# Optimization experiments

Hardware: AMD Instinct MI355X
Metric: run time of the kernel (lower is better)

## Reference

```python
import jax, jax.numpy as jnp
import numpy as np

N_EMBD = 1024
N_HEAD = 16
B, T = 4, 2048

def setup_inputs() -> dict:
    key = jax.random.key(0)
    ks = jax.random.split(key, 5)
    C = N_EMBD
    s = 0.02
    return {
        "x": jax.random.normal(ks[0], (B, T, C), dtype=jnp.float32),
        "W_attn": jax.random.normal(ks[1], (C, 3 * C), dtype=jnp.float32) * s,
        "b_attn": jnp.zeros((3 * C,), dtype=jnp.float32),
        "W_proj": jax.random.normal(ks[2], (C, C), dtype=jnp.float32) * s,
        "b_proj": jnp.zeros((C,), dtype=jnp.float32),
    }

def reference(x, W_attn, b_attn, W_proj, b_proj):
    Bz, Tz, C = x.shape
    H = N_HEAD
    hd = C // H
    qkv = x @ W_attn + b_attn                      # [B,T,3C]
    q, k, v = jnp.split(qkv, 3, axis=-1)
    # [B,H,T,hd]
    q = q.reshape(Bz, Tz, H, hd).transpose(0, 2, 1, 3)
    k = k.reshape(Bz, Tz, H, hd).transpose(0, 2, 1, 3)
    v = v.reshape(Bz, Tz, H, hd).transpose(0, 2, 1, 3)
    att = jnp.einsum('bhqd,bhkd->bhqk', q, k) * (1.0 / np.sqrt(hd))
    causal = jnp.tril(jnp.ones((Tz, Tz), dtype=bool))
    att = jnp.where(causal, att, -jnp.inf)
    att = jax.nn.softmax(att, axis=-1)
    y = jnp.einsum('bhqk,bhkd->bhqd', att, v)      # [B,H,T,hd]
    y = y.transpose(0, 2, 1, 3).reshape(Bz, Tz, C)
    return y @ W_proj + b_proj
```

## Files before the change

kernel.cpp:

```cpp
#include <hip/hip_runtime.h>
#include <hip/hip_bf16.h>

#define NEMBD 1024
#define NHEAD 16
#define HD    64
#define BB    4
#define TT    2048
#define MM    (BB*TT)
#define NQKV  (3*NEMBD)

typedef unsigned short u16;
typedef __attribute__((ext_vector_type(8))) short short8;
typedef __attribute__((ext_vector_type(4))) float floatx4;
typedef __attribute__((ext_vector_type(16))) float floatx16;

__device__ __forceinline__ u16 f2bf(float f) {
    __hip_bfloat16 h = __float2bfloat16(f);
    return *reinterpret_cast<u16*>(&h);
}

__device__ __forceinline__ unsigned pack_bf16(float a, float b) {
    __hip_bfloat162 h2 = __float22bfloat162_rn(float2{a, b});
    return *reinterpret_cast<unsigned*>(&h2);
}

__device__ __forceinline__ unsigned trunc_pack(float a, float b) {
    return __builtin_amdgcn_perm(__float_as_uint(b), __float_as_uint(a), 0x07060302u);
}

__device__ __forceinline__ void gl_lds16(const u16* g, u16* l) {
    __builtin_amdgcn_global_load_lds(
        (const __attribute__((address_space(1))) unsigned int*)g,
        (__attribute__((address_space(3))) unsigned int*)l,
        16, 0, 0);
}

__device__ __forceinline__ short8 scale8(short8 f, float c) {
    union { short8 s; unsigned u[4]; } a, r;
    a.s = f;
    for (int i = 0; i < 4; i++) {
        float lo = __uint_as_float(a.u[i] << 16) * c;
        float hi = __uint_as_float(a.u[i] & 0xffff0000u) * c;
        r.u[i] = pack_bf16(lo, hi);
    }
    return r.s;
}

__global__ __launch_bounds__(256) void cast_f32_bf16(const float* __restrict__ in,
                                                     u16* __restrict__ out, int n) {
    int i = (blockIdx.x * 256 + threadIdx.x) * 4;
    if (i < n) {
        float4 v = *(const float4*)(in + i);
        uint2 o;
        o.x = pack_bf16(v.x, v.y);
        o.y = pack_bf16(v.z, v.w);
        *(uint2*)(out + i) = o;
    }
}

__global__ __launch_bounds__(256) void transpose_cast(const float* __restrict__ in,
                                                      u16* __restrict__ out, int K, int N) {
    __shared__ float tile[32][33];
    int n0 = blockIdx.x * 32, k0 = blockIdx.y * 32;
    int tx = threadIdx.x, ty = threadIdx.y;
    for (int i = 0; i < 4; i++)
        tile[ty + i * 8][tx] = in[(k0 + ty + i * 8) * N + n0 + tx];
    __syncthreads();
    for (int i = 0; i < 4; i++)
        out[(n0 + ty + i * 8) * K + k0 + tx] = f2bf(tile[tx][ty + i * 8]);
}

template <int EPI>
__global__ __launch_bounds__(256)
void gemm_bt(const u16* __restrict__ A, const u16* __restrict__ Bt,
             const float* __restrict__ bias, void* __restrict__ out0,
             u16* __restrict__ outK, u16* __restrict__ outV) {
    const int K = NEMBD;
    __shared__ u16 As[128 * 64];
    __shared__ u16 Bs[128 * 64];
    int tid = threadIdx.x;
    int lane = tid & 63, w = tid >> 6;
    int l32 = lane & 31, lhi = lane >> 5;
    int wm = w >> 1, wn = w & 1;
    int bM = blockIdx.y * 128, bN = blockIdx.x * 128;

    floatx16 acc[2][2];
    for (int i = 0; i < 2; i++)
        for (int j = 0; j < 2; j++)
            acc[i][j] = (floatx16)(0.f);

    int srow = lane >> 3;
    int scol = ((lane & 7) ^ srow) * 8;
    const u16* Ag = A  + (size_t)(bM + w * 32 + srow) * K + scol;
    const u16* Bg = Bt + (size_t)(bN + w * 32 + srow) * K + scol;

    int physo[4];
    for (int kc = 0; kc < 4; kc++)
        physo[kc] = ((kc * 2 + lhi) ^ (lane & 7)) * 8;

    for (int k0 = 0; k0 < K; k0 += 64) {
        for (int i = 0; i < 4; i++) {
            gl_lds16(Ag + (size_t)i * 8 * K + k0, &As[(w * 32 + i * 8) * 64]);
            gl_lds16(Bg + (size_t)i * 8 * K + k0, &Bs[(w * 32 + i * 8) * 64]);
        }
        __syncthreads();
        for (int kc = 0; kc < 4; kc++) {
            short8 af[2], bf[2];
            for (int i = 0; i < 2; i++)
                af[i] = *(const short8*)&As[(wm * 64 + i * 32 + l32) * 64 + physo[kc]];
            for (int j = 0; j < 2; j++)
                bf[j] = *(const short8*)&Bs[(wn * 64 + j * 32 + l32) * 64 + physo[kc]];
            for (int i = 0; i < 2; i++)
                for (int j = 0; j < 2; j++)
                    acc[i][j] = __builtin_amdgcn_mfma_f32_32x32x16_bf16(af[i], bf[j], acc[i][j], 0, 0, 0);
        }
        __syncthreads();
    }

    for (int j = 0; j < 2; j++) {
        int n = bN + wn * 64 + j * 32 + l32;
        float bv = bias[n];
        for (int i = 0; i < 2; i++) {
            int mbase = bM + wm * 64 + i * 32 + 4 * lhi;
            for (int reg = 0; reg < 16; reg++) {
                float v = acc[i][j][reg] + bv;
                int mg = mbase + (reg & 3) + 8 * (reg >> 2);
                if (EPI == 0) {
                    int which = n >> 10, c = n & 1023;
                    int h = c >> 6, d = c & 63;
                    int b = mg >> 11, t = mg & 2047;
                    u16* dst = (which == 0) ? (u16*)out0 : (which == 1 ? outK : outV);
                    dst[(((size_t)(b * NHEAD + h) * TT) + t) * HD + d] = f2bf(v);
                } else {
                    ((float*)out0)[(size_t)mg * NEMBD + n] = v;
                }
            }
        }
    }
}

__global__ __launch_bounds__(256, 2)
void attn_kernel(const u16* __restrict__ Q, const u16* __restrict__ Kg,
                 const u16* __restrict__ V, u16* __restrict__ Y) {
    __shared__ u16 Ks[64][72];
    __shared__ u16 Vt[64][72];
    __shared__ u16 Ps[4][32][72];

    int tid = threadIdx.x;
    int lane = tid & 63, w = tid >> 6;
    int quad = lane >> 4, l16 = lane & 15;
    int bh = blockIdx.x;
    int jq = blockIdx.y;
    int q0 = jq * 128;
    const u16* Qb = Q  + (size_t)bh * TT * HD;
    const u16* Kb = Kg + (size_t)bh * TT * HD;
    const u16* Vb = V  + (size_t)bh * TT * HD;
    int wq = q0 + w * 32;

    const float C = 0.18033688f;

    short8 qf[2][2];
    for (int qt = 0; qt < 2; qt++)
        for (int kd = 0; kd < 2; kd++)
            qf[qt][kd] = scale8(*(const short8*)(Qb + (size_t)(wq + qt * 16 + l16) * HD + kd * 32 + quad * 8), C);

    floatx4 o[4][2];
    for (int dt = 0; dt < 4; dt++)
        for (int qt = 0; qt < 2; qt++)
            o[dt][qt] = (floatx4){0.f, 0.f, 0.f, 0.f};
    float l_s[2] = {0.f, 0.f};

    int krow = tid >> 2, kcg = (tid & 3) * 16;
    int vkp = (tid & 31) * 2, vd0 = (tid >> 5) * 8;

    auto stage_write = [&](uint4 k0v, uint4 k1v, uint4 v0, uint4 v1) {
        *(uint4*)&Ks[krow][kcg]     = k0v;
        *(uint4*)&Ks[krow][kcg + 8] = k1v;
        const unsigned* w0p = (const unsigned*)&v0;
        const unsigned* w1p = (const unsigned*)&v1;
        for (int e = 0; e < 4; e++) {
            *(unsigned*)&Vt[vd0 + 2 * e][vkp]     = __builtin_amdgcn_perm(w1p[e], w0p[e], 0x05040100u);
            *(unsigned*)&Vt[vd0 + 2 * e + 1][vkp] = __builtin_amdgcn_perm(w1p[e], w0p[e], 0x07060302u);
        }
    };

    auto process = [&](int k0) {
        short8 kf[4][2];
        for (int kt = 0; kt < 4; kt++)
            for (int kd = 0; kd < 2; kd++)
                kf[kt][kd] = *(const short8*)&Ks[kt * 16 + l16][kd * 32 + quad * 8];

        floatx4 s[2][4];
        for (int qt = 0; qt < 2; qt++)
            for (int kt = 0; kt < 4; kt++) {
                floatx4 a = (floatx4){0.f, 0.f, 0.f, 0.f};
                a = __builtin_amdgcn_mfma_f32_16x16x32_bf16(kf[kt][0], qf[qt][0], a, 0, 0, 0);
                a = __builtin_amdgcn_mfma_f32_16x16x32_bf16(kf[kt][1], qf[qt][1], a, 0, 0, 0);
                s[qt][kt] = a;
            }

        bool diag = (k0 + 64 > wq);
        for (int qt = 0; qt < 2; qt++) {
            int qg = wq + qt * 16 + l16;
            if (diag) {
                for (int kt = 0; kt < 4; kt++)
                    for (int r = 0; r < 4; r++)
                        if (k0 + kt * 16 + quad * 4 + r > qg) s[qt][kt][r] = -INFINITY;
            }
            float rs = 0.f;
            for (int kt = 0; kt < 4; kt++)
                for (int r = 0; r < 4; r++) {
                    float p = exp2f(s[qt][kt][r]);
                    s[qt][kt][r] = p;
                    rs += p;
                }
            l_s[qt] += rs;
        }

        for (int qt = 0; qt < 2; qt++)
            for (int kt = 0; kt < 4; kt++) {
                floatx4 p = s[qt][kt];
                *(unsigned*)&Ps[w][qt * 16 + l16][kt * 16 + quad * 4]     = trunc_pack(p[0], p[1]);
                *(unsigned*)&Ps[w][qt * 16 + l16][kt * 16 + quad * 4 + 2] = trunc_pack(p[2], p[3]);
            }
        short8 pfrag[2][2];
        for (int qt = 0; qt < 2; qt++)
            for (int c = 0; c < 2; c++)
                pfrag[qt][c] = *(const short8*)&Ps[w][qt * 16 + l16][c * 32 + quad * 8];
        for (int c = 0; c < 2; c++)
            for (int dt = 0; dt < 4; dt++) {
                short8 vfrag = *(const short8*)&Vt[dt * 16 + l16][c * 32 + quad * 8];
                for (int qt = 0; qt < 2; qt++)
                    o[dt][qt] = __builtin_amdgcn_mfma_f32_16x16x32_bf16(vfrag, pfrag[qt][c], o[dt][qt], 0, 0, 0);
            }
    };

    {
        uint4 k0v = *(const uint4*)(Kb + (size_t)krow * HD + kcg);
        uint4 k1v = *(const uint4*)(Kb + (size_t)krow * HD + kcg + 8);
        uint4 v0  = *(const uint4*)(Vb + (size_t)vkp * HD + vd0);
        uint4 v1  = *(const uint4*)(Vb + (size_t)(vkp + 1) * HD + vd0);
        stage_write(k0v, k1v, v0, v1);
    }
    __syncthreads();

    int kend = q0 + 128;
    for (int k0 = 0; k0 < kend; k0 += 64) {
        bool pref = (k0 + 64 < kend);
        uint4 nk0, nk1, nv0, nv1;
        if (pref) {
            nk0 = *(const uint4*)(Kb + (size_t)(k0 + 64 + krow) * HD + kcg);
            nk1 = *(const uint4*)(Kb + (size_t)(k0 + 64 + krow) * HD + kcg + 8);
            nv0 = *(const uint4*)(Vb + (size_t)(k0 + 64 + vkp) * HD + vd0);
            nv1 = *(const uint4*)(Vb + (size_t)(k0 + 64 + vkp + 1) * HD + vd0);
        }

        if (k0 < wq + 32) process(k0);

        __syncthreads();
        if (pref) {
            stage_write(nk0, nk1, nv0, nv1);
        }
        __syncthreads();
    }

    int b = bh >> 4, h = bh & 15;
    for (int qt = 0; qt < 2; qt++) {
        float lt = l_s[qt];
        lt += __shfl_xor(lt, 16, 64);
        lt += __shfl_xor(lt, 32, 64);
        float inv = 1.0f / lt;
        int qg = wq + qt * 16 + l16;
        size_t base = ((size_t)(b * TT + qg)) * NEMBD + h * HD;
        for (int dt = 0; dt < 4; dt++) {
            *(unsigned*)&Y[base + dt * 16 + quad * 4]     = pack_bf16(o[dt][qt][0] * inv, o[dt][qt][1] * inv);
            *(unsigned*)&Y[base + dt * 16 + quad * 4 + 2] = pack_bf16(o[dt][qt][2] * inv, o[dt][qt][3] * inv);
        }
    }
}

extern "C" void kernel_launch(void* const* d_in, const int* in_sizes, int n_in,
                              void* d_out, int out_size, void* d_ws, size_t ws_size,
                              hipStream_t stream) {
    const float* x      = (const float*)d_in[0];
    const float* W_attn = (const float*)d_in[1];
    const float* b_attn = (const float*)d_in[2];
    const float* W_proj = (const float*)d_in[3];
    const float* b_proj = (const float*)d_in[4];
    float* out = (float*)d_out;

    char* ws = (char*)d_ws;
    u16* xb  = (u16*)(ws + 0);
    u16* wat = (u16*)(ws + 16777216);
    u16* wpt = (u16*)(ws + 23068672);
    u16* Qb  = (u16*)(ws + 25165824);
    u16* Kb  = (u16*)(ws + 41943040);
    u16* Vb  = (u16*)(ws + 58720256);

    cast_f32_bf16<<<(MM * NEMBD / 4 + 255) / 256, 256, 0, stream>>>(x, xb, MM * NEMBD);
    dim3 tb(32, 8);
    transpose_cast<<<dim3(NQKV / 32, NEMBD / 32), tb, 0, stream>>>(W_attn, wat, NEMBD, NQKV);
    transpose_cast<<<dim3(NEMBD / 32, NEMBD / 32), tb, 0, stream>>>(W_proj, wpt, NEMBD, NEMBD);

    gemm_bt<0><<<dim3(NQKV / 128, MM / 128), 256, 0, stream>>>(xb, wat, b_attn, (void*)Qb, Kb, Vb);
    attn_kernel<<<dim3(BB * NHEAD, 16), 256, 0, stream>>>(Qb, Kb, Vb, xb);
    gemm_bt<1><<<dim3(NEMBD / 128, MM / 128), 256, 0, stream>>>(xb, wpt, b_proj, (void*)out, nullptr, nullptr);
}
```

Measured before the change: 254.2 us.

## Use 32x32 MFMA in attention, keep P in registers, double-buffer K/V

Rewrites the attention inner loop to use 32x32x16 bf16 MFMA tiles, so each wave handles 32 queries as a single tile. The probability matrix is repacked in registers with cross-lane shuffles instead of going through an LDS round-trip. K/V staging now uses two LDS buffers, which removes one barrier per iteration. The intent is to cut LDS traffic, barriers and MFMA issue count, at the cost of more accumulator registers and shuffle work.

Result: slower. 276.4 us (+8.7%).

```diff
diff --git a/kernel.cpp b/kernel.cpp
--- a/kernel.cpp
+++ b/kernel.cpp
@@ -26,6 +26,15 @@
 
 __device__ __forceinline__ unsigned trunc_pack(float a, float b) {
     return __builtin_amdgcn_perm(__float_as_uint(b), __float_as_uint(a), 0x07060302u);
+}
+
+__device__ __forceinline__ void plswap(unsigned &x, unsigned &y) {
+    unsigned xp = (unsigned)__shfl_xor((int)x, 32, 64);
+    unsigned yp = (unsigned)__shfl_xor((int)y, 32, 64);
+    bool hi = (threadIdx.x & 32) != 0;
+    unsigned nx = hi ? yp : x;
+    unsigned ny = hi ? y : xp;
+    x = nx; y = ny;
 }
 
 __device__ __forceinline__ void gl_lds16(const u16* g, u16* l) {
@@ -142,13 +151,12 @@
 __global__ __launch_bounds__(256, 2)
 void attn_kernel(const u16* __restrict__ Q, const u16* __restrict__ Kg,
                  const u16* __restrict__ V, u16* __restrict__ Y) {
-    __shared__ u16 Ks[64][72];
-    __shared__ u16 Vt[64][72];
-    __shared__ u16 Ps[4][32][72];
+    __shared__ u16 Ks[2][64][72];
+    __shared__ u16 Vt[2][64][72];
 
     int tid = threadIdx.x;
     int lane = tid & 63, w = tid >> 6;
-    int quad = lane >> 4, l16 = lane & 15;
+    int l32 = lane & 31, lhi = lane >> 5;
     int bh = blockIdx.x;
     int jq = blockIdx.y;
     int q0 = jq * 128;
@@ -156,83 +164,83 @@
     const u16* Kb = Kg + (size_t)bh * TT * HD;
     const u16* Vb = V  + (size_t)bh * TT * HD;
     int wq = q0 + w * 32;
+    int qg = wq + l32;
 
     const float C = 0.18033688f;
 
-    short8 qf[2][2];
-    for (int qt = 0; qt < 2; qt++)
-        for (int kd = 0; kd < 2; kd++)
-            qf[qt][kd] = scale8(*(const short8*)(Qb + (size_t)(wq + qt * 16 + l16) * HD + kd * 32 + quad * 8), C);
-
-    floatx4 o[4][2];
-    for (int dt = 0; dt < 4; dt++)
-        for (int qt = 0; qt < 2; qt++)
-            o[dt][qt] = (floatx4){0.f, 0.f, 0.f, 0.f};
-    float l_s[2] = {0.f, 0.f};
+    short8 qf[4];
+    for (int c = 0; c < 4; c++)
+        qf[c] = scale8(*(const short8*)(Qb + (size_t)qg * HD + c * 16 + lhi * 8), C);
+
+    floatx16 o[2];
+    o[0] = (floatx16)(0.f);
+    o[1] = (floatx16)(0.f);
+    float l_s = 0.f;
 
     int krow = tid >> 2, kcg = (tid & 3) * 16;
     int vkp = (tid & 31) * 2, vd0 = (tid >> 5) * 8;
 
-    auto stage_write = [&](uint4 k0v, uint4 k1v, uint4 v0, uint4 v1) {
-        *(uint4*)&Ks[krow][kcg]     = k0v;
-        *(uint4*)&Ks[krow][kcg + 8] = k1v;
+    auto stage_write = [&](int bp, uint4 k0v, uint4 k1v, uint4 v0, uint4 v1) {
+        *(uint4*)&Ks[bp][krow][kcg]     = k0v;
+        *(uint4*)&Ks[bp][krow][kcg + 8] = k1v;
         const unsigned* w0p = (const unsigned*)&v0;
         const unsigned* w1p = (const unsigned*)&v1;
         for (int e = 0; e < 4; e++) {
-            *(unsigned*)&Vt[vd0 + 2 * e][vkp]     = __builtin_amdgcn_perm(w1p[e], w0p[e], 0x05040100u);
-            *(unsigned*)&Vt[vd0 + 2 * e + 1][vkp] = __builtin_amdgcn_perm(w1p[e], w0p[e], 0x07060302u);
+            *(unsigned*)&Vt[bp][vd0 + 2 * e][vkp]     = __builtin_amdgcn_perm(w1p[e], w0p[e], 0x05040100u);
+            *(unsigned*)&Vt[bp][vd0 + 2 * e + 1][vkp] = __builtin_amdgcn_perm(w1p[e], w0p[e], 0x07060302u);
         }
     };
 
-    auto process = [&](int k0) {
-        short8 kf[4][2];
-        for (int kt = 0; kt < 4; kt++)
-            for (int kd = 0; kd < 2; kd++)
-                kf[kt][kd] = *(const short8*)&Ks[kt * 16 + l16][kd * 32 + quad * 8];
-
-        floatx4 s[2][4];
-        for (int qt = 0; qt < 2; qt++)
-            for (int kt = 0; kt < 4; kt++) {
-                floatx4 a = (floatx4){0.f, 0.f, 0.f, 0.f};
-                a = __builtin_amdgcn_mfma_f32_16x16x32_bf16(kf[kt][0], qf[qt][0], a, 0, 0, 0);
-                a = __builtin_amdgcn_mfma_f32_16x16x32_bf16(kf[kt][1], qf[qt][1], a, 0, 0, 0);
-                s[qt][kt] = a;
+    auto process = [&](int k0, int bp) {
+        floatx16 s[2];
+        s[0] = (floatx16)(0.f);
+        s[1] = (floatx16)(0.f);
+#pragma unroll
+        for (int c = 0; c < 4; c++) {
+            short8 kf0 = *(const short8*)&Ks[bp][l32][c * 16 + lhi * 8];
+            short8 kf1 = *(const short8*)&Ks[bp][32 + l32][c * 16 + lhi * 8];
+            s[0] = __builtin_amdgcn_mfma_f32_32x32x16_bf16(kf0, qf[c], s[0], 0, 0, 0);
+            s[1] = __builtin_amdgcn_mfma_f32_32x32x16_bf16(kf1, qf[c], s[1], 0, 0, 0);
+        }
+
+        bool diag = (k0 + 64 > wq);
+        float rs = 0.f;
+#pragma unroll
+        for (int t = 0; t < 2; t++)
+#pragma unroll
+            for (int r = 0; r < 16; r++) {
+                if (diag) {
+                    int kg = k0 + t * 32 + (r & 3) + 8 * (r >> 2) + 4 * lhi;
+                    if (kg > qg) s[t][r] = -INFINITY;
+                }
+                float p = exp2f(s[t][r]);
+                s[t][r] = p;
+                rs += p;
             }
-
-        bool diag = (k0 + 64 > wq);
-        for (int qt = 0; qt < 2; qt++) {
-            int qg = wq + qt * 16 + l16;
-            if (diag) {
-                for (int kt = 0; kt < 4; kt++)
-                    for (int r = 0; r < 4; r++)
-                        if (k0 + kt * 16 + quad * 4 + r > qg) s[qt][kt][r] = -INFINITY;
-            }
-            float rs = 0.f;
-            for (int kt = 0; kt < 4; kt++)
-                for (int r = 0; r < 4; r++) {
-                    float p = exp2f(s[qt][kt][r]);
-                    s[qt][kt][r] = p;
-                    rs += p;
-                }
-            l_s[qt] += rs;
-        }
-
-        for (int qt = 0; qt < 2; qt++)
-            for (int kt = 0; kt < 4; kt++) {
-                floatx4 p = s[qt][kt];
-                *(unsigned*)&Ps[w][qt * 16 + l16][kt * 16 + quad * 4]     = trunc_pack(p[0], p[1]);
-                *(unsigned*)&Ps[w][qt * 16 + l16][kt * 16 + quad * 4 + 2] = trunc_pack(p[2], p[3]);
-            }
-        short8 pfrag[2][2];
-        for (int qt = 0; qt < 2; qt++)
-            for (int c = 0; c < 2; c++)
-                pfrag[qt][c] = *(const short8*)&Ps[w][qt * 16 + l16][c * 32 + quad * 8];
-        for (int c = 0; c < 2; c++)
-            for (int dt = 0; dt < 4; dt++) {
-                short8 vfrag = *(const short8*)&Vt[dt * 16 + l16][c * 32 + quad * 8];
-                for (int qt = 0; qt < 2; qt++)
-                    o[dt][qt] = __builtin_amdgcn_mfma_f32_16x16x32_bf16(vfrag, pfrag[qt][c], o[dt][qt], 0, 0, 0);
-            }
+        l_s += rs;
+
+        short8 pfrag[4];
+#pragma unroll
+        for (int kc = 0; kc < 4; kc++) {
+            const int t = kc >> 1, h0 = (kc & 1) * 8;
+            unsigned pa = trunc_pack(s[t][h0 + 0], s[t][h0 + 1]);
+            unsigned pb = trunc_pack(s[t][h0 + 2], s[t][h0 + 3]);
+            unsigned pc = trunc_pack(s[t][h0 + 4], s[t][h0 + 5]);
+            unsigned pd = trunc_pack(s[t][h0 + 6], s[t][h0 + 7]);
+            plswap(pa, pc);
+            plswap(pb, pd);
+            union { unsigned u[4]; short8 s8; } pf;
+            pf.u[0] = pa; pf.u[1] = pb; pf.u[2] = pc; pf.u[3] = pd;
+            pfrag[kc] = pf.s8;
+        }
+
+#pragma unroll
+        for (int kc = 0; kc < 4; kc++) {
+            short8 vf0 = *(const short8*)&Vt[bp][l32][kc * 16 + lhi * 8];
+            short8 vf1 = *(const short8*)&Vt[bp][32 + l32][kc * 16 + lhi * 8];
+            o[0] = __builtin_amdgcn_mfma_f32_32x32x16_bf16(vf0, pfrag[kc], o[0], 0, 0, 0);
+            o[1] = __builtin_amdgcn_mfma_f32_32x32x16_bf16(vf1, pfrag[kc], o[1], 0, 0, 0);
+        }
     };
 
     {
@@ -240,12 +248,13 @@
         uint4 k1v = *(const uint4*)(Kb + (size_t)krow * HD + kcg + 8);
         uint4 v0  = *(const uint4*)(Vb + (size_t)vkp * HD + vd0);
         uint4 v1  = *(const uint4*)(Vb + (size_t)(vkp + 1) * HD + vd0);
-        stage_write(k0v, k1v, v0, v1);
+        stage_write(0, k0v, k1v, v0, v1);
     }
     __syncthreads();
 
     int kend = q0 + 128;
-    for (int k0 = 0; k0 < kend; k0 += 64) {
+    int p = 0;
+    for (int k0 = 0; k0 < kend; k0 += 64, p ^= 1) {
         bool pref = (k0 + 64 < kend);
         uint4 nk0, nk1, nv0, nv1;
         if (pref) {
@@ -255,28 +264,24 @@
             nv1 = *(const uint4*)(Vb + (size_t)(k0 + 64 + vkp + 1) * HD + vd0);
         }
 
-        if (k0 < wq + 32) process(k0);
-
+        if (k0 < wq + 32) process(k0, p);
+
+        if (pref) stage_write(p ^ 1, nk0, nk1, nv0, nv1);
         __syncthreads();
-        if (pref) {
-            stage_write(nk0, nk1, nv0, nv1);
-        }
-        __syncthreads();
-    }
-
+    }
+
+    float lt = l_s + __shfl_xor(l_s, 32, 64);
+    float inv = 1.0f / lt;
     int b = bh >> 4, h = bh & 15;
-    for (int qt = 0; qt < 2; qt++) {
-        float lt = l_s[qt];
-        lt += __shfl_xor(lt, 16, 64);
-        lt += __shfl_xor(lt, 32, 64);
-        float inv = 1.0f / lt;
-        int qg = wq + qt * 16 + l16;
-        size_t base = ((size_t)(b * TT + qg)) * NEMBD + h * HD;
-        for (int dt = 0; dt < 4; dt++) {
-            *(unsigned*)&Y[base + dt * 16 + quad * 4]     = pack_bf16(o[dt][qt][0] * inv, o[dt][qt][1] * inv);
-            *(unsigned*)&Y[base + dt * 16 + quad * 4 + 2] = pack_bf16(o[dt][qt][2] * inv, o[dt][qt][3] * inv);
-        }
-    }
+    size_t base = ((size_t)(b * TT + qg)) * NEMBD + h * HD;
+    for (int dt = 0; dt < 2; dt++)
+        for (int g = 0; g < 4; g++) {
+            int d0 = dt * 32 + g * 8 + lhi * 4;
+            uint2 ov;
+            ov.x = pack_bf16(o[dt][g * 4 + 0] * inv, o[dt][g * 4 + 1] * inv);
+            ov.y = pack_bf16(o[dt][g * 4 + 2] * inv, o[dt][g * 4 + 3] * inv);
+            *(uint2*)&Y[base + d0] = ov;
+        }
 }
 
 extern "C" void kernel_launch(void* const* d_in, const int* in_sizes, int n_in,
```
